# Kernel optimization log

Measured on AMD Instinct MI355X. Metric: run time of the kernel, lower is better.

The kernel has to match this reference:

```python
import jax, jax.numpy as jnp
import numpy as np

EMB = 128
EDGE = 32
STEPS = 3


def _lrelu(x):
    return jax.nn.leaky_relu(x, negative_slope=0.01)


def setup_inputs() -> dict:
    key = jax.random.key(0)
    ks = jax.random.split(key, 16)
    N, E, G = 50000, 400000, 256
    x = jax.random.normal(ks[0], (N, EMB), jnp.float32)
    edge_attr = jax.random.normal(ks[1], (E, EDGE), jnp.float32)
    edge_index = jax.random.randint(ks[2], (2, E), 0, N, jnp.int64)
    batch_ind = jnp.sort(jax.random.randint(ks[3], (N,), 0, G, jnp.int64))
    data_lens = jax.random.randint(ks[4], (G,), 0, G, jnp.int64)
    s = 1.0 / np.sqrt(EMB)
    Wm = jax.random.normal(ks[5], (STEPS, EMB + EDGE, EMB), jnp.float32) * s
    bm = jnp.zeros((STEPS, EMB), jnp.float32)
    Wa = jax.random.normal(ks[6], (STEPS, 3 * EMB, EMB), jnp.float32) * s
    ba = jnp.zeros((STEPS, EMB), jnp.float32)
    Wgate = jax.random.normal(ks[7], (STEPS, EMB), jnp.float32) * s
    bgate = jnp.zeros((STEPS,), jnp.float32)
    Wfeat = jax.random.normal(ks[8], (STEPS, EMB, EMB), jnp.float32) * s
    bfeat = jnp.zeros((STEPS, EMB), jnp.float32)
    Wt = jax.random.normal(ks[9], (STEPS, 2 * EMB, EMB), jnp.float32) * s
    bt = jnp.zeros((STEPS, EMB), jnp.float32)
    return {"x": x, "edge_attr": edge_attr, "Wm": Wm, "bm": bm, "Wa": Wa,
            "ba": ba, "Wgate": Wgate, "bgate": bgate, "Wfeat": Wfeat,
            "bfeat": bfeat, "Wt": Wt, "bt": bt, "edge_index": edge_index,
            "batch_ind": batch_ind, "num_graphs": 256, "data_lens": data_lens}


def reference(x, edge_attr, Wm, bm, Wa, ba, Wgate, bgate, Wfeat, bfeat, Wt, bt,
              edge_index, batch_ind, num_graphs, data_lens):
    N = x.shape[0]
    src, dst = edge_index[0], edge_index[1]  # PyG: x_j = x[src], aggregate at dst
    xg = jnp.zeros((num_graphs, EMB), x.dtype)  # xg_init is None -> zeros
    for s in range(STEPS):
        # GraphNet: gather -> message MLP -> scatter-max -> update MLP + residual
        xg_node = xg[batch_ind]                                   # [N, emb]
        z = jnp.concatenate([x[src], edge_attr], axis=1)          # [E, emb+edge]
        m = _lrelu(z @ Wm[s] + bm[s])                             # [E, emb]
        agg = jax.ops.segment_max(m, dst, num_segments=N)         # [N, emb]
        agg = jnp.where(jnp.isneginf(agg), 0.0, agg)              # PyG fills empty with 0
        z2 = jnp.concatenate([x, xg_node, agg], axis=1)           # [N, 3*emb]
        x = _lrelu(z2 @ Wa[s] + ba[s]) + x
        # GlobalNode: segment-softmax attention pooling + transform + residual
        gate = x @ Wgate[s] + bgate[s]                            # [N]
        gmax = jax.ops.segment_max(gate, batch_ind, num_segments=num_graphs)
        gmax = jnp.where(jnp.isneginf(gmax), 0.0, gmax)
        e = jnp.exp(gate - gmax[batch_ind])
        denom = jax.ops.segment_sum(e, batch_ind, num_segments=num_graphs)
        alpha = e / denom[batch_ind]                              # [N]
        feat = _lrelu(x @ Wfeat[s] + bfeat[s])                    # [N, emb]
        pooled = jax.ops.segment_sum(alpha[:, None] * feat, batch_ind,
                                     num_segments=num_graphs)     # [G, emb]
        cat = jnp.concatenate([pooled, xg], axis=1)               # [G, 2*emb]
        xg = _lrelu(cat @ Wt[s] + bt[s]) + xg
    return x, xg
```

## Files before the change

kernel.cpp:

```cpp
#include <hip/hip_runtime.h>
#include <hip/hip_bf16.h>

#define EMB 128
#define EDGE 32
#define STEPS 3

typedef short bf8s __attribute__((ext_vector_type(8)));
typedef float f32x4 __attribute__((ext_vector_type(4)));

__device__ __forceinline__ float lrelu(float v) { return v > 0.0f ? v : 0.01f * v; }
__device__ __forceinline__ unsigned short f2bf(float f) {
    unsigned u = __float_as_uint(f);
    u += 0x7fffu + ((u >> 16) & 1u);
    return (unsigned short)(u >> 16);
}
__device__ __forceinline__ float bf2f(unsigned short s) {
    return __uint_as_float(((unsigned)s) << 16);
}
__device__ __forceinline__ unsigned pk2bf(float x, float y) {
    __hip_bfloat162 h = __float22bfloat162_rn(make_float2(x, y));
    return *(unsigned*)&h;
}

__global__ void k_hist(const int* __restrict__ dst, int E, int* __restrict__ deg) {
    int e = blockIdx.x * 256 + threadIdx.x;
    if (e < E) atomicAdd(&deg[dst[e]], 1);
}

__global__ void k_scan1(const int* __restrict__ deg, int N, int* __restrict__ rowptr,
                        int* __restrict__ bsums) {
    __shared__ int s[256];
    int t = threadIdx.x;
    int i = blockIdx.x * 256 + t;
    int v = (i < N) ? deg[i] : 0;
    s[t] = v;
    __syncthreads();
#pragma unroll
    for (int off = 1; off < 256; off <<= 1) {
        int x = (t >= off) ? s[t - off] : 0;
        __syncthreads();
        s[t] += x;
        __syncthreads();
    }
    if (i < N) rowptr[i] = s[t] - v;
    if (t == 255) bsums[blockIdx.x] = s[255];
}

__global__ void k_scan2(int* __restrict__ bsums, int NB) {
    __shared__ int s[256];
    __shared__ int carry;
    int t = threadIdx.x;
    if (t == 0) carry = 0;
    __syncthreads();
    for (int base = 0; base < NB; base += 256) {
        int i = base + t;
        int v = (i < NB) ? bsums[i] : 0;
        s[t] = v;
        __syncthreads();
#pragma unroll
        for (int off = 1; off < 256; off <<= 1) {
            int x = (t >= off) ? s[t - off] : 0;
            __syncthreads();
            s[t] += x;
            __syncthreads();
        }
        int excl = s[t] - v + carry;
        if (i < NB) bsums[i] = excl;
        int tot = s[255];
        __syncthreads();
        if (t == 0) carry += tot;
        __syncthreads();
    }
}

__global__ void k_scan3(int* __restrict__ rowptr, const int* __restrict__ bsums, int N, int E) {
    int i = blockIdx.x * 256 + threadIdx.x;
    if (i < N) rowptr[i] += bsums[i >> 8];
    if (i == 0) rowptr[N] = E;
}

__global__ void k_fill(const int* __restrict__ src, const int* __restrict__ dst, int E,
                       int* __restrict__ cursor, int2* __restrict__ sp2) {
    int e = blockIdx.x * 256 + threadIdx.x;
    if (e >= E) return;
    int d = dst[e];
    int p = atomicAdd(&cursor[d], 1);
    sp2[p] = make_int2(src[e], e);
}

__global__ __launch_bounds__(256) void k_eaperm(const float* __restrict__ ea,
                                                const int2* __restrict__ sp2,
                                                unsigned short* __restrict__ ea16p,
                                                int* __restrict__ srcp, int E) {
    int p = blockIdx.x * 256 + threadIdx.x;
    if (p >= E) return;
    int2 sp = sp2[p];
    srcp[p] = sp.x;
    const float4* er = (const float4*)(ea + (size_t)sp.y * EDGE);
    union { unsigned u[16]; int4 v[4]; } o;
#pragma unroll
    for (int q = 0; q < 8; ++q) {
        float4 v = er[q];
        o.u[2 * q]     = pk2bf(v.x, v.y);
        o.u[2 * q + 1] = pk2bf(v.z, v.w);
    }
    int4* dp = (int4*)(ea16p + (size_t)p * EDGE);
#pragma unroll
    for (int q = 0; q < 4; ++q) dp[q] = o.v[q];
}

__global__ void k_hsent(unsigned short* __restrict__ h, int N) {
    h[(size_t)N * EMB + threadIdx.x] = 0xFF80u;
}

__global__ void k_gb0(const float* __restrict__ ba, float* __restrict__ gb) {
    gb[(size_t)blockIdx.x * EMB + threadIdx.x] = ba[threadIdx.x];
}

__global__ void k_gstart(const int* __restrict__ batch, int N, int G, int* __restrict__ gstart) {
    int g = blockIdx.x * blockDim.x + threadIdx.x;
    if (g > G) return;
    int lo = 0, hi = N;
    while (lo < hi) {
        int mid = (lo + hi) >> 1;
        if (batch[mid] < g) lo = mid + 1; else hi = mid;
    }
    gstart[g] = lo;
}

__global__ __launch_bounds__(256) void k_wpack(const float* __restrict__ Wm,
                                               const float* __restrict__ Wa,
                                               const float* __restrict__ Wfeat,
                                               unsigned short* __restrict__ wpack) {
    int gid = blockIdx.x * 256 + threadIdx.x;
    int unit = gid >> 14;
    int e = gid & 16383;
    int s = unit / 5, u = unit % 5;
    const float* src; int rows;
    switch (u) {
        case 0: src = Wm + (size_t)s * 160 * EMB;             rows = 128; break;
        case 1: src = Wm + (size_t)s * 160 * EMB + 128 * EMB; rows = 32;  break;
        case 2: src = Wa + (size_t)s * 384 * EMB;             rows = 128; break;
        case 3: src = Wa + (size_t)s * 384 * EMB + 256 * EMB; rows = 128; break;
        default: src = Wfeat + (size_t)s * EMB * EMB;         rows = 128; break;
    }
    int k = e >> 7, n = e & 127;
    if (k >= rows) return;
    unsigned short b = f2bf(src[(size_t)k * EMB + n]);
    int kc = k >> 5, c = n >> 4, lane = (n & 15) | (((k & 31) >> 3) << 4), j = k & 7;
    wpack[(size_t)unit * 16384 + ((size_t)(kc * 8 + c) * 64 + lane) * 8 + j] = b;
}

__device__ __forceinline__ void loadAx(const float* __restrict__ A, int row0, int wv,
                                       int lane, int N, bf8s af[4]) {
    int li = lane & 15, oct = lane >> 4;
    int m = row0 + wv * 16 + li;
    if (m >= N) m = N - 1;
    const float4* xr = (const float4*)(A + (size_t)m * EMB);
#pragma unroll
    for (int kc = 0; kc < 4; ++kc) {
        float4 a0 = xr[kc * 8 + oct * 2];
        float4 a1 = xr[kc * 8 + oct * 2 + 1];
        union { bf8s v; unsigned u[4]; } c;
        c.u[0] = pk2bf(a0.x, a0.y);
        c.u[1] = pk2bf(a0.z, a0.w);
        c.u[2] = pk2bf(a1.x, a1.y);
        c.u[3] = pk2bf(a1.z, a1.w);
        af[kc] = c.v;
    }
}
__device__ __forceinline__ void loadAa(const unsigned short* __restrict__ A16, int row0,
                                       int wv, int lane, int N, bf8s af[4]) {
    int li = lane & 15, oct = lane >> 4;
    int m = row0 + wv * 16 + li;
    if (m >= N) m = N - 1;
    const bf8s* ar = (const bf8s*)(A16 + (size_t)m * EMB);
#pragma unroll
    for (int kc = 0; kc < 4; ++kc) af[kc] = ar[kc * 4 + oct];
}
__device__ __forceinline__ void stageB(const unsigned short* __restrict__ Bp,
                                       unsigned short* lB, int tid) {
#pragma unroll
    for (int i = 0; i < 8; ++i) {
        int idx = tid + i * 256;
        ((int4*)lB)[idx] = ((const int4*)Bp)[idx];
    }
}
__device__ __forceinline__ void mfma128r(const bf8s af[4], const unsigned short* lB,
                                         f32x4 acc[8], int lane) {
#pragma unroll
    for (int kc = 0; kc < 4; ++kc) {
#pragma unroll
        for (int c = 0; c < 8; ++c) {
            bf8s b = *(const bf8s*)&lB[((kc * 8 + c) * 64 + lane) * 8];
            acc[c] = __builtin_amdgcn_mfma_f32_16x16x32_bf16(af[kc], b, acc[c], 0, 0, 0);
        }
    }
}

__global__ __launch_bounds__(256) void k_gemm_bias(const float* __restrict__ A,
                                                   const unsigned short* __restrict__ Bp,
                                                   const float* __restrict__ bias,
                                                   unsigned short* __restrict__ C, int N) {
    __shared__ unsigned short lB[16384];
    int tid = threadIdx.x, wv = tid >> 6, lane = tid & 63;
    int row0 = blockIdx.x * 64;
    stageB(Bp, lB, tid);
    bf8s af[4];
    loadAx(A, row0, wv, lane, N, af);
    __syncthreads();
    f32x4 acc[8];
#pragma unroll
    for (int c = 0; c < 8; ++c) acc[c] = (f32x4){0.f, 0.f, 0.f, 0.f};
    mfma128r(af, lB, acc, lane);
    int li = lane & 15, quad = lane >> 4;
    float bcol[8];
#pragma unroll
    for (int c = 0; c < 8; ++c) bcol[c] = bias[c * 16 + li];
#pragma unroll
    for (int rr = 0; rr < 4; ++rr) {
        int m = row0 + wv * 16 + quad * 4 + rr;
        if (m < N) {
            union { bf8s v; unsigned u[4]; } o;
#pragma unroll
            for (int j = 0; j < 4; ++j)
                o.u[j] = pk2bf(acc[2 * j][rr] + bcol[2 * j],
                               acc[2 * j + 1][rr] + bcol[2 * j + 1]);
            *(bf8s*)&C[(size_t)m * EMB + li * 8] = o.v;
        }
    }
}

__global__ __launch_bounds__(256) void k_gemm_node(const float* __restrict__ x,
                                                   const unsigned short* __restrict__ agg16,
                                                   const unsigned short* __restrict__ BpX,
                                                   const unsigned short* __restrict__ BpA,
                                                   const float* __restrict__ gb,
                                                   const int* __restrict__ batch,
                                                   float* __restrict__ xout,
                                                   const float* __restrict__ wg,
                                                   const float* __restrict__ bg,
                                                   float* __restrict__ gate, int N) {
    __shared__ unsigned short lB[16384];
    int tid = threadIdx.x, wv = tid >> 6, lane = tid & 63;
    int row0 = blockIdx.x * 64;
    stageB(BpX, lB, tid);
    bf8s af[4];
    loadAx(x, row0, wv, lane, N, af);
    __syncthreads();
    f32x4 acc[8];
#pragma unroll
    for (int c = 0; c < 8; ++c) acc[c] = (f32x4){0.f, 0.f, 0.f, 0.f};
    mfma128r(af, lB, acc, lane);
    __syncthreads();
    stageB(BpA, lB, tid);
    loadAa(agg16, row0, wv, lane, N, af);
    __syncthreads();
    mfma128r(af, lB, acc, lane);
    int li = lane & 15, quad = lane >> 4;
    float gpart[4] = {0.f, 0.f, 0.f, 0.f};
#pragma unroll
    for (int c = 0; c < 8; ++c) {
        int col = c * 16 + li;
        float wgc = wg[col];
#pragma unroll
        for (int rr = 0; rr < 4; ++rr) {
            int m = row0 + wv * 16 + quad * 4 + rr;
            if (m < N) {
                int g = batch[m];
                float b = gb[(size_t)g * EMB + col];
                float res = x[(size_t)m * EMB + col];
                float v = lrelu(acc[c][rr] + b) + res;
                xout[(size_t)m * EMB + col] = v;
                gpart[rr] = fmaf(v, wgc, gpart[rr]);
            }
        }
    }
#pragma unroll
    for (int rr = 0; rr < 4; ++rr) {
#pragma unroll
        for (int off = 1; off < 16; off <<= 1)
            gpart[rr] += __shfl_xor(gpart[rr], off, 64);
    }
    if (li == 0) {
        float b0 = bg[0];
#pragma unroll
        for (int rr = 0; rr < 4; ++rr) {
            int m = row0 + wv * 16 + quad * 4 + rr;
            if (m < N) gate[m] = gpart[rr] + b0;
        }
    }
}

__global__ __launch_bounds__(256) void k_gemm_feat(const float* __restrict__ A,
                                                   const unsigned short* __restrict__ Bp,
                                                   const float* __restrict__ bias,
                                                   const float* __restrict__ gate,
                                                   const float* __restrict__ gmax,
                                                   const float* __restrict__ denom,
                                                   const int* __restrict__ batch,
                                                   float* __restrict__ pooled, int N) {
    __shared__ unsigned short lB[16384];
    int tid = threadIdx.x, wv = tid >> 6, lane = tid & 63;
    int row0 = blockIdx.x * 64;
    stageB(Bp, lB, tid);
    bf8s af[4];
    loadAx(A, row0, wv, lane, N, af);
    __syncthreads();
    f32x4 acc[8];
#pragma unroll
    for (int c = 0; c < 8; ++c) acc[c] = (f32x4){0.f, 0.f, 0.f, 0.f};
    mfma128r(af, lB, acc, lane);
    int li = lane & 15, quad = lane >> 4;
    int rb = row0 + wv * 16;
    if (rb >= N) return;
    float alpha[4];
    int grow[4];
#pragma unroll
    for (int rr = 0; rr < 4; ++rr) {
        int m = rb + quad * 4 + rr;
        if (m < N) {
            int g = batch[m];
            grow[rr] = g;
            alpha[rr] = __expf(gate[m] - gmax[g]) / denom[g];
        } else { alpha[rr] = 0.f; grow[rr] = 0; }
    }
    int gs = batch[rb];
    int mlast = rb + 15; if (mlast >= N) mlast = N - 1;
    bool uni = (gs == batch[mlast]);
#pragma unroll
    for (int c = 0; c < 8; ++c) {
        int col = c * 16 + li;
        float b = bias[col];
        float v0 = alpha[0] * lrelu(acc[c][0] + b);
        float v1 = alpha[1] * lrelu(acc[c][1] + b);
        float v2 = alpha[2] * lrelu(acc[c][2] + b);
        float v3 = alpha[3] * lrelu(acc[c][3] + b);
        if (uni) {
            float s = (v0 + v1) + (v2 + v3);
            s += __shfl_xor(s, 16, 64);
            s += __shfl_xor(s, 32, 64);
            if (quad == 0) atomicAdd(&pooled[(size_t)gs * EMB + col], s);
        } else {
            if (rb + quad * 4 + 0 < N) atomicAdd(&pooled[(size_t)grow[0] * EMB + col], v0);
            if (rb + quad * 4 + 1 < N) atomicAdd(&pooled[(size_t)grow[1] * EMB + col], v1);
            if (rb + quad * 4 + 2 < N) atomicAdd(&pooled[(size_t)grow[2] * EMB + col], v2);
            if (rb + quad * 4 + 3 < N) atomicAdd(&pooled[(size_t)grow[3] * EMB + col], v3);
        }
    }
}

__global__ __launch_bounds__(256) void k_gseg(const float* __restrict__ gate,
                                              const int* __restrict__ gstart,
                                              float* __restrict__ gmax,
                                              float* __restrict__ denom,
                                              float* __restrict__ pooled) {
    int g = blockIdx.x;
    int t = threadIdx.x;
    if (t < EMB) pooled[(size_t)g * EMB + t] = 0.f;
    int s0 = gstart[g], s1 = gstart[g + 1];
    __shared__ float red[256];
    float mx = -__builtin_inff();
    for (int i = s0 + t; i < s1; i += 256) mx = fmaxf(mx, gate[i]);
    red[t] = mx;
    __syncthreads();
#pragma unroll
    for (int off = 128; off; off >>= 1) {
        if (t < off) red[t] = fmaxf(red[t], red[t + off]);
        __syncthreads();
    }
    float m = red[0];
    __syncthreads();
    float sum = 0.f;
    for (int i = s0 + t; i < s1; i += 256) sum += __expf(gate[i] - m);
    red[t] = sum;
    __syncthreads();
#pragma unroll
    for (int off = 128; off; off >>= 1) {
        if (t < off) red[t] += red[t + off];
        __syncthreads();
    }
    if (t == 0) {
        gmax[g] = (s1 > s0) ? m : 0.f;
        denom[g] = red[0];
    }
}

__global__ __launch_bounds__(128) void k_xg(const float* __restrict__ pooled,
                                            const float* __restrict__ xg,
                                            const float* __restrict__ Wt,
                                            const float* __restrict__ bt,
                                            float* __restrict__ xg_out,
                                            const float* __restrict__ WaGn,
                                            const float* __restrict__ ban,
                                            float* __restrict__ gb) {
    int g = blockIdx.x, c = threadIdx.x;
    __shared__ float row[256];
    row[c] = pooled[(size_t)g * EMB + c];
    row[c + 128] = xg[(size_t)g * EMB + c];
    __syncthreads();
    float acc = bt[c];
#pragma unroll 8
    for (int k = 0; k < 256; ++k) acc = fmaf(row[k], Wt[(size_t)k * EMB + c], acc);
    float v = lrelu(acc) + row[c + 128];
    xg_out[(size_t)g * EMB + c] = v;
    if (WaGn) {
        __syncthreads();
        row[c] = v;
        __syncthreads();
        float a2 = ban[c];
#pragma unroll 8
        for (int k = 0; k < EMB; ++k) a2 = fmaf(row[k], WaGn[(size_t)k * EMB + c], a2);
        gb[(size_t)g * EMB + c] = a2;
    }
}

__global__ __launch_bounds__(256) void k_fagg(const unsigned short* __restrict__ h,
                                              const unsigned short* __restrict__ ea16p,
                                              const int* __restrict__ srcp,
                                              const int* __restrict__ rowptr,
                                              const unsigned short* __restrict__ Bp,
                                              unsigned short* __restrict__ agg, int N) {
    __shared__ unsigned short lB[4096];
    int tid = threadIdx.x;
    ((int4*)lB)[tid]       = ((const int4*)Bp)[tid];
    ((int4*)lB)[tid + 256] = ((const int4*)Bp)[tid + 256];
    __syncthreads();
    int wv = tid >> 6, lane = tid & 63;
    int n = blockIdx.x * 4 + wv;
    if (n >= N) return;
    int li = lane & 15, oct = lane >> 4;
    int r0 = rowptr[n], r1 = rowptr[n + 1], deg = r1 - r0;

    float vm[8];
#pragma unroll
    for (int ci = 0; ci < 8; ++ci) vm[ci] = -__builtin_inff();

    for (int b = 0; b < deg; b += 16) {
        int p = r0 + b + li;
        if (p > r1 - 1) p = r1 - 1;
        int srcv = srcp[p];
        bf8s a = *(const bf8s*)&ea16p[(size_t)p * EDGE + oct * 8];
        union { bf8s v; unsigned short s[8]; } hv[4];
#pragma unroll
        for (int rr = 0; rr < 4; ++rr) {
            int sr = __shfl(srcv, oct * 4 + rr, 16);
            if (b + oct * 4 + rr >= deg) sr = N;
            hv[rr].v = *(const bf8s*)&h[(size_t)sr * EMB + li * 8];
        }
#pragma unroll
        for (int ci = 0; ci < 8; ++ci) {
            bf8s bb = *(const bf8s*)&lB[(ci * 64 + lane) * 8];
            f32x4 acc;
            acc[0] = bf2f(hv[0].s[ci]);
            acc[1] = bf2f(hv[1].s[ci]);
            acc[2] = bf2f(hv[2].s[ci]);
            acc[3] = bf2f(hv[3].s[ci]);
            acc = __builtin_amdgcn_mfma_f32_16x16x32_bf16(a, bb, acc, 0, 0, 0);
#pragma unroll
            for (int rr = 0; rr < 4; ++rr) vm[ci] = fmaxf(vm[ci], acc[rr]);
        }
    }
#pragma unroll
    for (int ci = 0; ci < 8; ++ci) {
        vm[ci] = fmaxf(vm[ci], __shfl_xor(vm[ci], 16, 64));
        vm[ci] = fmaxf(vm[ci], __shfl_xor(vm[ci], 32, 64));
    }
    float s0 = (oct == 0) ? vm[0] : (oct == 1) ? vm[1] : (oct == 2) ? vm[2] : vm[3];
    float s1 = (oct == 0) ? vm[4] : (oct == 1) ? vm[5] : (oct == 2) ? vm[6] : vm[7];
    s0 = lrelu(s0);
    s1 = lrelu(s1);
    if (deg == 0) { s0 = 0.f; s1 = 0.f; }
    agg[(size_t)n * EMB + oct * 16 + li]        = f2bf(s0);
    agg[(size_t)n * EMB + (oct + 4) * 16 + li]  = f2bf(s1);
}

extern "C" void kernel_launch(void* const* d_in, const int* in_sizes, int n_in,
                              void* d_out, int out_size, void* d_ws, size_t ws_size,
                              hipStream_t stream) {
    const float* x0    = (const float*)d_in[0];
    const float* ea    = (const float*)d_in[1];
    const float* Wm    = (const float*)d_in[2];
    const float* bm    = (const float*)d_in[3];
    const float* Wa    = (const float*)d_in[4];
    const float* ba    = (const float*)d_in[5];
    const float* Wgate = (const float*)d_in[6];
    const float* bgate = (const float*)d_in[7];
    const float* Wfeat = (const float*)d_in[8];
    const float* bfeat = (const float*)d_in[9];
    const float* Wt    = (const float*)d_in[10];
    const float* bt    = (const float*)d_in[11];
    const int*   eidx  = (const int*)d_in[12];
    const int*   batch = (const int*)d_in[13];

    int N = in_sizes[0] / EMB;
    int E = in_sizes[1] / EDGE;
    int G = in_sizes[15];

    char* w = (char*)d_ws;
    auto alloc = [&](size_t bytes) {
        char* p = w;
        w += (bytes + 255) & ~(size_t)255;
        return p;
    };
    unsigned short* h16   = (unsigned short*)alloc((size_t)(N + 1) * EMB * 2);
    unsigned short* agg16 = (unsigned short*)alloc((size_t)N * EMB * 2);
    float* gate   = (float*)alloc((size_t)N * 4);
    float* gb     = (float*)alloc((size_t)G * EMB * 4);
    float* pooled = (float*)alloc((size_t)G * EMB * 4);
    float* gmax   = (float*)alloc((size_t)G * 4);
    float* denom  = (float*)alloc((size_t)G * 4);
    float* xg_a   = (float*)alloc((size_t)G * EMB * 4);
    float* xg_b   = (float*)alloc((size_t)G * EMB * 4);
    int* deg      = (int*)alloc((size_t)N * 4);
    int* rowptr   = (int*)alloc((size_t)(N + 1) * 4);
    int* cursor   = (int*)alloc((size_t)N * 4);
    int2* sp2     = (int2*)alloc((size_t)E * 8);
    int* srcp     = (int*)alloc((size_t)E * 4);
    unsigned short* ea16p = (unsigned short*)alloc((size_t)E * EDGE * 2);
    int* gstart   = (int*)alloc((size_t)(G + 1) * 4);
    int* bsums    = (int*)alloc(1024 * 4);
    unsigned short* wpack = (unsigned short*)alloc((size_t)15 * 16384 * 2);

    const int* esrc = eidx;
    const int* edst = eidx + E;
    int ebl = (E + 255) / 256;
    int NB  = (N + 255) / 256;

    hipMemsetAsync(deg, 0, (size_t)N * 4, stream);
    k_hist<<<ebl, 256, 0, stream>>>(edst, E, deg);
    k_scan1<<<NB, 256, 0, stream>>>(deg, N, rowptr, bsums);
    k_scan2<<<1, 256, 0, stream>>>(bsums, NB);
    k_scan3<<<NB, 256, 0, stream>>>(rowptr, bsums, N, E);
    hipMemcpyAsync(cursor, rowptr, (size_t)N * 4, hipMemcpyDeviceToDevice, stream);
    k_fill<<<ebl, 256, 0, stream>>>(esrc, edst, E, cursor, sp2);
    k_eaperm<<<ebl, 256, 0, stream>>>(ea, sp2, ea16p, srcp, E);
    k_hsent<<<1, 128, 0, stream>>>(h16, N);
    k_gb0<<<G, 128, 0, stream>>>(ba, gb);
    k_gstart<<<(G + 256) / 256, 256, 0, stream>>>(batch, N, G, gstart);
    hipMemsetAsync(xg_a, 0, (size_t)G * EMB * 4, stream);
    k_wpack<<<960, 256, 0, stream>>>(Wm, Wa, Wfeat, wpack);

    int gemm_blocks = (N + 63) / 64;
    int fagg_blocks = (N + 3) / 4;

    const float* x_in = x0;
    float* xg_cur = xg_a;
    float* xg_nxt = xg_b;

    for (int s = 0; s < STEPS; ++s) {
        const unsigned short* wp = wpack + (size_t)s * 5 * 16384;
        float* x_out = (s == STEPS - 1) ? (float*)d_out : (float*)x_in;

        k_gemm_bias<<<gemm_blocks, 256, 0, stream>>>(x_in, wp + 0 * 16384, bm + s * EMB,
                                                     h16, N);
        k_fagg<<<fagg_blocks, 256, 0, stream>>>(h16, ea16p, srcp, rowptr, wp + 1 * 16384,
                                                agg16, N);
        k_gemm_node<<<gemm_blocks, 256, 0, stream>>>(x_in, agg16, wp + 2 * 16384,
                                                     wp + 3 * 16384, gb, batch, x_out,
                                                     Wgate + s * EMB, bgate + s, gate, N);
        k_gseg<<<G, 256, 0, stream>>>(gate, gstart, gmax, denom, pooled);
        k_gemm_feat<<<gemm_blocks, 256, 0, stream>>>(x_out, wp + 4 * 16384, bfeat + s * EMB,
                                                     gate, gmax, denom, batch, pooled, N);
        const float* WaGn = (s < STEPS - 1) ? Wa + (size_t)(s + 1) * 384 * EMB + 128 * EMB
                                            : nullptr;
        const float* ban  = (s < STEPS - 1) ? ba + (s + 1) * EMB : nullptr;
        k_xg<<<G, 128, 0, stream>>>(pooled, xg_cur, Wt + (size_t)s * 256 * EMB,
                                    bt + s * EMB, xg_nxt, WaGn, ban, gb);

        x_in = x_out;
        float* tmp = xg_cur; xg_cur = xg_nxt; xg_nxt = tmp;
    }

    hipMemcpyAsync((float*)d_out + (size_t)N * EMB, xg_cur, (size_t)G * EMB * 4,
                   hipMemcpyDeviceToDevice, stream);
}
```

Baseline: 559.6 us.

## Keep a bf16 shadow copy of node features and merge setup kernels

```diff
diff --git a/kernel.cpp b/kernel.cpp
--- a/kernel.cpp
+++ b/kernel.cpp
@@ -73,9 +73,14 @@
     }
 }
 
-__global__ void k_scan3(int* __restrict__ rowptr, const int* __restrict__ bsums, int N, int E) {
+__global__ void k_scan3(int* __restrict__ rowptr, const int* __restrict__ bsums,
+                        int* __restrict__ cursor, int N, int E) {
     int i = blockIdx.x * 256 + threadIdx.x;
-    if (i < N) rowptr[i] += bsums[i >> 8];
+    if (i < N) {
+        int v = rowptr[i] + bsums[i >> 8];
+        rowptr[i] = v;
+        cursor[i] = v;
+    }
     if (i == 0) rowptr[N] = E;
 }
 
@@ -109,23 +114,53 @@
     for (int q = 0; q < 4; ++q) dp[q] = o.v[q];
 }
 
-__global__ void k_hsent(unsigned short* __restrict__ h, int N) {
-    h[(size_t)N * EMB + threadIdx.x] = 0xFF80u;
-}
-
-__global__ void k_gb0(const float* __restrict__ ba, float* __restrict__ gb) {
-    gb[(size_t)blockIdx.x * EMB + threadIdx.x] = ba[threadIdx.x];
-}
-
-__global__ void k_gstart(const int* __restrict__ batch, int N, int G, int* __restrict__ gstart) {
-    int g = blockIdx.x * blockDim.x + threadIdx.x;
-    if (g > G) return;
-    int lo = 0, hi = N;
-    while (lo < hi) {
-        int mid = (lo + hi) >> 1;
-        if (batch[mid] < g) lo = mid + 1; else hi = mid;
-    }
-    gstart[g] = lo;
+__global__ __launch_bounds__(256) void k_setup(const float* __restrict__ x0,
+                                               unsigned short* __restrict__ x16,
+                                               int N, int XB, int NB,
+                                               const float* __restrict__ ba,
+                                               float* __restrict__ gb,
+                                               float* __restrict__ xg_a,
+                                               const int* __restrict__ batch,
+                                               int* __restrict__ gstart, int G,
+                                               unsigned short* __restrict__ h16,
+                                               int* __restrict__ deg) {
+    int b = blockIdx.x, t = threadIdx.x;
+    if (b < XB) {
+        size_t idx = ((size_t)b * 256 + t) * 8;
+        if (idx < (size_t)N * EMB) {
+            const float4* s = (const float4*)(x0 + idx);
+            float4 v0 = s[0], v1 = s[1];
+            union { bf8s v; unsigned u[4]; } o;
+            o.u[0] = pk2bf(v0.x, v0.y);
+            o.u[1] = pk2bf(v0.z, v0.w);
+            o.u[2] = pk2bf(v1.x, v1.y);
+            o.u[3] = pk2bf(v1.z, v1.w);
+            *(bf8s*)(x16 + idx) = o.v;
+        }
+        return;
+    }
+    b -= XB;
+    if (b < NB) {
+        int i = b * 256 + t;
+        if (i < N) deg[i] = 0;
+        return;
+    }
+    b -= NB;
+    if (b < G) {
+        if (t < EMB) gb[(size_t)b * EMB + t] = ba[t];
+        else xg_a[(size_t)b * EMB + (t - EMB)] = 0.f;
+        if (t == 0) {
+            int lo = 0, hi = N;
+            while (lo < hi) {
+                int mid = (lo + hi) >> 1;
+                if (batch[mid] < b) lo = mid + 1; else hi = mid;
+            }
+            gstart[b] = lo;
+        }
+        return;
+    }
+    if (t < EMB) h16[(size_t)N * EMB + t] = 0xFF80u;
+    if (t == EMB) gstart[G] = N;
 }
 
 __global__ __launch_bounds__(256) void k_wpack(const float* __restrict__ Wm,
@@ -151,24 +186,6 @@
     wpack[(size_t)unit * 16384 + ((size_t)(kc * 8 + c) * 64 + lane) * 8 + j] = b;
 }
 
-__device__ __forceinline__ void loadAx(const float* __restrict__ A, int row0, int wv,
-                                       int lane, int N, bf8s af[4]) {
-    int li = lane & 15, oct = lane >> 4;
-    int m = row0 + wv * 16 + li;
-    if (m >= N) m = N - 1;
-    const float4* xr = (const float4*)(A + (size_t)m * EMB);
-#pragma unroll
-    for (int kc = 0; kc < 4; ++kc) {
-        float4 a0 = xr[kc * 8 + oct * 2];
-        float4 a1 = xr[kc * 8 + oct * 2 + 1];
-        union { bf8s v; unsigned u[4]; } c;
-        c.u[0] = pk2bf(a0.x, a0.y);
-        c.u[1] = pk2bf(a0.z, a0.w);
-        c.u[2] = pk2bf(a1.x, a1.y);
-        c.u[3] = pk2bf(a1.z, a1.w);
-        af[kc] = c.v;
-    }
-}
 __device__ __forceinline__ void loadAa(const unsigned short* __restrict__ A16, int row0,
                                        int wv, int lane, int N, bf8s af[4]) {
     int li = lane & 15, oct = lane >> 4;
@@ -198,7 +215,7 @@
     }
 }
 
-__global__ __launch_bounds__(256) void k_gemm_bias(const float* __restrict__ A,
+__global__ __launch_bounds__(256) void k_gemm_bias(const unsigned short* __restrict__ A16,
                                                    const unsigned short* __restrict__ Bp,
                                                    const float* __restrict__ bias,
                                                    unsigned short* __restrict__ C, int N) {
@@ -207,7 +224,7 @@
     int row0 = blockIdx.x * 64;
     stageB(Bp, lB, tid);
     bf8s af[4];
-    loadAx(A, row0, wv, lane, N, af);
+    loadAa(A16, row0, wv, lane, N, af);
     __syncthreads();
     f32x4 acc[8];
 #pragma unroll
@@ -232,6 +249,7 @@
 }
 
 __global__ __launch_bounds__(256) void k_gemm_node(const float* __restrict__ x,
+                                                   unsigned short* __restrict__ x16,
                                                    const unsigned short* __restrict__ agg16,
                                                    const unsigned short* __restrict__ BpX,
                                                    const unsigned short* __restrict__ BpA,
@@ -246,7 +264,7 @@
     int row0 = blockIdx.x * 64;
     stageB(BpX, lB, tid);
     bf8s af[4];
-    loadAx(x, row0, wv, lane, N, af);
+    loadAa(x16, row0, wv, lane, N, af);
     __syncthreads();
     f32x4 acc[8];
 #pragma unroll
@@ -272,6 +290,7 @@
                 float res = x[(size_t)m * EMB + col];
                 float v = lrelu(acc[c][rr] + b) + res;
                 xout[(size_t)m * EMB + col] = v;
+                x16[(size_t)m * EMB + col] = f2bf(v);
                 gpart[rr] = fmaf(v, wgc, gpart[rr]);
             }
         }
@@ -292,7 +311,7 @@
     }
 }
 
-__global__ __launch_bounds__(256) void k_gemm_feat(const float* __restrict__ A,
+__global__ __launch_bounds__(256) void k_gemm_feat(const unsigned short* __restrict__ A16,
                                                    const unsigned short* __restrict__ Bp,
                                                    const float* __restrict__ bias,
                                                    const float* __restrict__ gate,
@@ -305,7 +324,7 @@
     int row0 = blockIdx.x * 64;
     stageB(Bp, lB, tid);
     bf8s af[4];
-    loadAx(A, row0, wv, lane, N, af);
+    loadAa(A16, row0, wv, lane, N, af);
     __syncthreads();
     f32x4 acc[8];
 #pragma unroll
@@ -415,19 +434,18 @@
     }
 }
 
-__global__ __launch_bounds__(256) void k_fagg(const unsigned short* __restrict__ h,
-                                              const unsigned short* __restrict__ ea16p,
-                                              const int* __restrict__ srcp,
-                                              const int* __restrict__ rowptr,
-                                              const unsigned short* __restrict__ Bp,
-                                              unsigned short* __restrict__ agg, int N) {
+__global__ __launch_bounds__(1024) void k_fagg(const unsigned short* __restrict__ h,
+                                               const unsigned short* __restrict__ ea16p,
+                                               const int* __restrict__ srcp,
+                                               const int* __restrict__ rowptr,
+                                               const unsigned short* __restrict__ Bp,
+                                               unsigned short* __restrict__ agg, int N) {
     __shared__ unsigned short lB[4096];
     int tid = threadIdx.x;
-    ((int4*)lB)[tid]       = ((const int4*)Bp)[tid];
-    ((int4*)lB)[tid + 256] = ((const int4*)Bp)[tid + 256];
+    if (tid < 512) ((int4*)lB)[tid] = ((const int4*)Bp)[tid];
     __syncthreads();
     int wv = tid >> 6, lane = tid & 63;
-    int n = blockIdx.x * 4 + wv;
+    int n = blockIdx.x * 16 + wv;
     if (n >= N) return;
     int li = lane & 15, oct = lane >> 4;
     int r0 = rowptr[n], r1 = rowptr[n + 1], deg = r1 - r0;
@@ -504,6 +522,7 @@
         return p;
     };
     unsigned short* h16   = (unsigned short*)alloc((size_t)(N + 1) * EMB * 2);
+    unsigned short* x16   = (unsigned short*)alloc((size_t)N * EMB * 2);
     unsigned short* agg16 = (unsigned short*)alloc((size_t)N * EMB * 2);
     float* gate   = (float*)alloc((size_t)N * 4);
     float* gb     = (float*)alloc((size_t)G * EMB * 4);
@@ -526,23 +545,20 @@
     const int* edst = eidx + E;
     int ebl = (E + 255) / 256;
     int NB  = (N + 255) / 256;
-
-    hipMemsetAsync(deg, 0, (size_t)N * 4, stream);
+    int XB  = ((size_t)N * EMB / 8 + 255) / 256;
+
+    k_setup<<<XB + NB + G + 1, 256, 0, stream>>>(x0, x16, N, XB, NB, ba, gb, xg_a,
+                                                 batch, gstart, G, h16, deg);
     k_hist<<<ebl, 256, 0, stream>>>(edst, E, deg);
     k_scan1<<<NB, 256, 0, stream>>>(deg, N, rowptr, bsums);
     k_scan2<<<1, 256, 0, stream>>>(bsums, NB);
-    k_scan3<<<NB, 256, 0, stream>>>(rowptr, bsums, N, E);
-    hipMemcpyAsync(cursor, rowptr, (size_t)N * 4, hipMemcpyDeviceToDevice, stream);
+    k_scan3<<<NB, 256, 0, stream>>>(rowptr, bsums, cursor, N, E);
     k_fill<<<ebl, 256, 0, stream>>>(esrc, edst, E, cursor, sp2);
     k_eaperm<<<ebl, 256, 0, stream>>>(ea, sp2, ea16p, srcp, E);
-    k_hsent<<<1, 128, 0, stream>>>(h16, N);
-    k_gb0<<<G, 128, 0, stream>>>(ba, gb);
-    k_gstart<<<(G + 256) / 256, 256, 0, stream>>>(batch, N, G, gstart);
-    hipMemsetAsync(xg_a, 0, (size_t)G * EMB * 4, stream);
     k_wpack<<<960, 256, 0, stream>>>(Wm, Wa, Wfeat, wpack);
 
     int gemm_blocks = (N + 63) / 64;
-    int fagg_blocks = (N + 3) / 4;
+    int fagg_blocks = (N + 15) / 16;
 
     const float* x_in = x0;
     float* xg_cur = xg_a;
@@ -552,15 +568,15 @@
         const unsigned short* wp = wpack + (size_t)s * 5 * 16384;
         float* x_out = (s == STEPS - 1) ? (float*)d_out : (float*)x_in;
 
-        k_gemm_bias<<<gemm_blocks, 256, 0, stream>>>(x_in, wp + 0 * 16384, bm + s * EMB,
+        k_gemm_bias<<<gemm_blocks, 256, 0, stream>>>(x16, wp + 0 * 16384, bm + s * EMB,
                                                      h16, N);
-        k_fagg<<<fagg_blocks, 256, 0, stream>>>(h16, ea16p, srcp, rowptr, wp + 1 * 16384,
-                                                agg16, N);
-        k_gemm_node<<<gemm_blocks, 256, 0, stream>>>(x_in, agg16, wp + 2 * 16384,
+        k_fagg<<<fagg_blocks, 1024, 0, stream>>>(h16, ea16p, srcp, rowptr, wp + 1 * 16384,
+                                                 agg16, N);
+        k_gemm_node<<<gemm_blocks, 256, 0, stream>>>(x_in, x16, agg16, wp + 2 * 16384,
                                                      wp + 3 * 16384, gb, batch, x_out,
                                                      Wgate + s * EMB, bgate + s, gate, N);
         k_gseg<<<G, 256, 0, stream>>>(gate, gstart, gmax, denom, pooled);
-        k_gemm_feat<<<gemm_blocks, 256, 0, stream>>>(x_out, wp + 4 * 16384, bfeat + s * EMB,
+        k_gemm_feat<<<gemm_blocks, 256, 0, stream>>>(x16, wp + 4 * 16384, bfeat + s * EMB,
                                                      gate, gmax, denom, batch, pooled, N);
         const float* WaGn = (s < STEPS - 1) ? Wa + (size_t)(s + 1) * 384 * EMB + 128 * EMB
                                             : nullptr;
```

Result: no change. 564.0 us (+0.8%).
